# Kernel tuning notes

Hardware: AMD Instinct MI355X
Metric: run time of the kernel (lower is better)

## Reference

```python
import jax, jax.numpy as jnp
import numpy as np

TEMPERATURE = 0.07

def l2norm(x, eps=1e-12):
    # torch.nn.functional.normalize(dim=1): x / max(||x||, eps)
    n = jnp.sqrt(jnp.sum(x * x, axis=1, keepdims=True))
    return x / jnp.maximum(n, eps)

def setup_inputs() -> dict:
    key = jax.random.key(0)
    ks = jax.random.split(key, 8)
    B, D_in, H, M, Q, NNEG = 1024, 2048, 1024, 256, 65536, 16384
    return {
        "y1": jax.random.normal(ks[0], (B, D_in), dtype=jnp.float32),
        "y2": jax.random.normal(ks[1], (B, D_in), dtype=jnp.float32),
        "W_enc_q": jax.random.normal(ks[2], (D_in, H), dtype=jnp.float32) * 0.02,
        "W_enc_k": jax.random.normal(ks[3], (D_in, H), dtype=jnp.float32) * 0.02,
        "W_proj": jax.random.normal(ks[4], (H, M), dtype=jnp.float32) * 0.02,
        "queue": jax.random.normal(ks[5], (Q, M), dtype=jnp.float32),
        "sample_idx": jax.random.randint(ks[6], (NNEG,), 0, Q, dtype=jnp.int32),
        "write_idx": jnp.arange(B, dtype=jnp.int32),
    }

def reference(y1, y2, W_enc_q, W_enc_k, W_proj, queue, sample_idx, write_idx):
    # query path (trainable)
    q = l2norm((y2 @ W_enc_q) @ W_proj)                 # [B, M]
    # key path (no_grad in original)
    k = jax.lax.stop_gradient(l2norm((y1 @ W_enc_k) @ W_proj))  # [B, M]
    # sample negatives from GPU-resident queue (gather) + normalize
    neg = l2norm(queue[sample_idx])                     # [NNEG, M]
    pos_logits = jnp.sum(q * k, axis=1, keepdims=True)  # [B, 1]
    neg_logits = q @ neg.T                              # [B, NNEG]
    logits = jnp.concatenate([pos_logits, neg_logits], axis=1) / TEMPERATURE
    # cross_entropy with labels == 0
    loss = -jnp.mean(jax.nn.log_softmax(logits, axis=-1)[:, 0])
    # FIFO append modeled as circular-buffer scatter write
    new_queue = queue.at[write_idx].set(k)
    return loss, new_queue
```

## Files before the change

### kernel.cpp

```cpp
#include <hip/hip_runtime.h>
#include <hip/hip_bf16.h>
#include <math.h>
#include <stdint.h>


typedef __attribute__((ext_vector_type(4))) float floatx4;
typedef __attribute__((ext_vector_type(8))) short bf16x8;
typedef __attribute__((ext_vector_type(8))) unsigned short ushort8;

#define BM 128
#define BN 128
#define BK 32

__device__ __forceinline__ unsigned short f2bf(float x) {
    union { float f; unsigned int u; } v; v.f = x;
    unsigned int r = v.u + 0x7FFFu + ((v.u >> 16) & 1u);
    return (unsigned short)(r >> 16);
}

__device__ __forceinline__ void async_cp16(const void* g, void* l) {
    auto gp = reinterpret_cast<const __attribute__((address_space(1))) unsigned int*>(
        reinterpret_cast<uintptr_t>(g));
    auto lp = reinterpret_cast<__attribute__((address_space(3))) unsigned int*>(
        reinterpret_cast<uintptr_t>(l));
    __builtin_amdgcn_global_load_lds(gp, lp, 16, 0, 0);
}

__global__ __launch_bounds__(256) void copy_f4(const float4* __restrict__ in,
                                               float4* __restrict__ out, int n4) {
    int i = blockIdx.x * 256 + threadIdx.x;
    int stride = gridDim.x * 256;
    for (; i < n4; i += stride) out[i] = in[i];
}

__global__ __launch_bounds__(256) void cast_bf16(const float* __restrict__ in,
                                                 unsigned short* __restrict__ out,
                                                 long n) {
    long i = (long)blockIdx.x * 256 + threadIdx.x;
    const float4* in4 = (const float4*)in;
    float4 a = in4[i * 2], b = in4[i * 2 + 1];
    ushort8 o;
    o[0] = f2bf(a.x); o[1] = f2bf(a.y); o[2] = f2bf(a.z); o[3] = f2bf(a.w);
    o[4] = f2bf(b.x); o[5] = f2bf(b.y); o[6] = f2bf(b.z); o[7] = f2bf(b.w);
    ((ushort8*)out)[i] = o;
}

__global__ __launch_bounds__(256) void transpose_cast(const float* __restrict__ in,
                                                      unsigned short* __restrict__ out,
                                                      int R, int C) {
    __shared__ unsigned short tile[32][33];
    int c0 = blockIdx.x * 32, r0 = blockIdx.y * 32;
    int tx = threadIdx.x & 31, ty = threadIdx.x >> 5;
#pragma unroll
    for (int i = 0; i < 4; ++i)
        tile[ty + i * 8][tx] = f2bf(in[(size_t)(r0 + ty + i * 8) * C + c0 + tx]);
    __syncthreads();
#pragma unroll
    for (int i = 0; i < 4; ++i)
        out[(size_t)(c0 + ty + i * 8) * R + r0 + tx] = tile[tx][ty + i * 8];
}

__global__ __launch_bounds__(256) void gemm_nt(const unsigned short* __restrict__ Ag,
                                               const unsigned short* __restrict__ Bg,
                                               float* __restrict__ Cg,
                                               int M_, int N_, int K_, int nsplit,
                                               long sAb, long sBb) {
    __shared__ unsigned short As[BM * BK];
    __shared__ unsigned short Bs[BN * BK];
    const int z = blockIdx.z;
    const int batch = z / nsplit, split = z - batch * nsplit;
    const unsigned short* A = Ag + (long)batch * sAb;
    const unsigned short* B = Bg + (long)batch * sBb;
    float* C = Cg + (long)z * M_ * N_;
    const int Kc = K_ / nsplit;
    const int kbeg = split * Kc;
    const int row0 = blockIdx.y * BM, col0 = blockIdx.x * BN;
    const int t = threadIdx.x;
    const int wave = t >> 6, lane = t & 63;
    const int wr = wave >> 1, wc = wave & 1;
    const int lrow = lane & 15, quad = lane >> 4;

    floatx4 acc[4][4] = {};

    for (int kk = kbeg; kk < kbeg + Kc; kk += BK) {
#pragma unroll
        for (int r = 0; r < 2; ++r) {
            int c = t + r * 256;
            int arow = c >> 2, aoff = (c & 3) * 8;
            async_cp16(A + (size_t)(row0 + arow) * K_ + kk + aoff,
                       (char*)As + (size_t)c * 16);
            async_cp16(B + (size_t)(col0 + arow) * K_ + kk + aoff,
                       (char*)Bs + (size_t)c * 16);
        }
        __syncthreads();
        bf16x8 af[4], bfr[4];
#pragma unroll
        for (int i = 0; i < 4; ++i) {
            af[i]  = *(const bf16x8*)(As + (size_t)(wr * 64 + i * 16 + lrow) * BK + quad * 8);
            bfr[i] = *(const bf16x8*)(Bs + (size_t)(wc * 64 + i * 16 + lrow) * BK + quad * 8);
        }
#pragma unroll
        for (int i = 0; i < 4; ++i)
#pragma unroll
            for (int j = 0; j < 4; ++j)
                acc[i][j] = __builtin_amdgcn_mfma_f32_16x16x32_bf16(af[i], bfr[j], acc[i][j], 0, 0, 0);
        __syncthreads();
    }
#pragma unroll
    for (int i = 0; i < 4; ++i) {
        int grow = row0 + wr * 64 + i * 16 + quad * 4;
#pragma unroll
        for (int j = 0; j < 4; ++j) {
            int gcol = col0 + wc * 64 + j * 16 + lrow;
#pragma unroll
            for (int r = 0; r < 4; ++r)
                C[(size_t)(grow + r) * N_ + gcol] = acc[i][j][r];
        }
    }
}

__global__ __launch_bounds__(256) void reduce2_cast(const float* __restrict__ P,
                                                    unsigned short* __restrict__ out,
                                                    long BH) {
    long i = ((long)blockIdx.x * 256 + threadIdx.x) * 8;
    long batch = (i >= BH) ? 1 : 0;
    long j = i - batch * BH;
    const float* p0 = P + batch * 2 * BH + j;
    const float* p1 = p0 + BH;
    float4 a0 = *(const float4*)p0, a1 = *(const float4*)(p0 + 4);
    float4 b0 = *(const float4*)p1, b1 = *(const float4*)(p1 + 4);
    ushort8 o;
    o[0] = f2bf(a0.x + b0.x); o[1] = f2bf(a0.y + b0.y);
    o[2] = f2bf(a0.z + b0.z); o[3] = f2bf(a0.w + b0.w);
    o[4] = f2bf(a1.x + b1.x); o[5] = f2bf(a1.y + b1.y);
    o[6] = f2bf(a1.z + b1.z); o[7] = f2bf(a1.w + b1.w);
    *(ushort8*)(out + i) = o;
}

__global__ __launch_bounds__(256) void qk_finalize(const float* __restrict__ P,
                                                   const int* __restrict__ widx,
                                                   unsigned short* __restrict__ qkb,
                                                   float* __restrict__ newq,
                                                   float* __restrict__ pos,
                                                   float* __restrict__ sumexp,
                                                   int B_, int nsplit, float invT) {
    const int i = blockIdx.x, t = threadIdx.x;
    const long RM = (long)B_ * 256;
    float sq = 0.f, sk = 0.f;
    for (int s = 0; s < nsplit; ++s) {
        sq += P[(long)s * RM + (long)i * 256 + t];
        sk += P[(long)(nsplit + s) * RM + (long)i * 256 + t];
    }
    __shared__ float r0[256], r1[256], r2[256];
    r0[t] = sq * sq; r1[t] = sk * sk; r2[t] = sq * sk;
    __syncthreads();
    for (int off = 128; off > 0; off >>= 1) {
        if (t < off) { r0[t] += r0[t + off]; r1[t] += r1[t + off]; r2[t] += r2[t + off]; }
        __syncthreads();
    }
    float nq = fmaxf(sqrtf(r0[0]), 1e-12f);
    float nk = fmaxf(sqrtf(r1[0]), 1e-12f);
    float qn = sq / nq, kn = sk / nk;
    qkb[(size_t)i * 256 + t] = f2bf(qn);
    qkb[(size_t)(B_ + i) * 256 + t] = f2bf(kn);
    newq[(size_t)widx[i] * 256 + t] = kn;
    if (t == 0) {
        float p = (r2[0] / (nq * nk)) * invT;
        pos[i] = p;
        sumexp[i] = __expf(p);
    }
}

__global__ __launch_bounds__(256) void gather_norm(const float* __restrict__ queue,
                                                   const int* __restrict__ sidx,
                                                   unsigned short* __restrict__ neg) {
    const int r = blockIdx.x * 4 + (threadIdx.x >> 6);
    const int lane = threadIdx.x & 63;
    const float4* src = (const float4*)(queue + (size_t)sidx[r] * 256);
    float4 v = src[lane];
    float ss = v.x * v.x + v.y * v.y + v.z * v.z + v.w * v.w;
#pragma unroll
    for (int off = 1; off < 64; off <<= 1) ss += __shfl_xor(ss, off);
    float inv = 1.f / fmaxf(sqrtf(ss), 1e-12f);
    ushort8 dummy; (void)dummy;
    unsigned short o[4] = { f2bf(v.x * inv), f2bf(v.y * inv),
                            f2bf(v.z * inv), f2bf(v.w * inv) };
    *(unsigned long long*)(neg + (size_t)r * 256 + lane * 4) =
        *(unsigned long long*)o;
}

__global__ __launch_bounds__(256) void gemm_logits(const unsigned short* __restrict__ A,
                                                   const unsigned short* __restrict__ B,
                                                   float* __restrict__ sumexp,
                                                   int N_, int K_, float invT) {
    __shared__ unsigned short As[BM * BK];
    __shared__ unsigned short Bs[BN * BK];
    __shared__ float rowred[BM];
    const int row0 = blockIdx.y * BM, col0 = blockIdx.x * BN;
    const int t = threadIdx.x;
    const int wave = t >> 6, lane = t & 63;
    const int wr = wave >> 1, wc = wave & 1;
    const int lrow = lane & 15, quad = lane >> 4;

    floatx4 acc[4][4] = {};

    for (int kk = 0; kk < K_; kk += BK) {
#pragma unroll
        for (int r = 0; r < 2; ++r) {
            int c = t + r * 256;
            int arow = c >> 2, aoff = (c & 3) * 8;
            async_cp16(A + (size_t)(row0 + arow) * K_ + kk + aoff,
                       (char*)As + (size_t)c * 16);
            async_cp16(B + (size_t)(col0 + arow) * K_ + kk + aoff,
                       (char*)Bs + (size_t)c * 16);
        }
        __syncthreads();
        bf16x8 af[4], bfr[4];
#pragma unroll
        for (int i = 0; i < 4; ++i) {
            af[i]  = *(const bf16x8*)(As + (size_t)(wr * 64 + i * 16 + lrow) * BK + quad * 8);
            bfr[i] = *(const bf16x8*)(Bs + (size_t)(wc * 64 + i * 16 + lrow) * BK + quad * 8);
        }
#pragma unroll
        for (int i = 0; i < 4; ++i)
#pragma unroll
            for (int j = 0; j < 4; ++j)
                acc[i][j] = __builtin_amdgcn_mfma_f32_16x16x32_bf16(af[i], bfr[j], acc[i][j], 0, 0, 0);
        __syncthreads();
    }
    if (t < BM) rowred[t] = 0.f;
    __syncthreads();
#pragma unroll
    for (int i = 0; i < 4; ++i) {
#pragma unroll
        for (int r = 0; r < 4; ++r) {
            float s = 0.f;
#pragma unroll
            for (int j = 0; j < 4; ++j) s += __expf(acc[i][j][r] * invT);
            s += __shfl_xor(s, 1); s += __shfl_xor(s, 2);
            s += __shfl_xor(s, 4); s += __shfl_xor(s, 8);
            if (lrow == 0) atomicAdd(&rowred[wr * 64 + i * 16 + quad * 4 + r], s);
        }
    }
    __syncthreads();
    if (t < BM) atomicAdd(&sumexp[row0 + t], rowred[t]);
}

__global__ __launch_bounds__(256) void final_loss(const float* __restrict__ pos,
                                                  const float* __restrict__ sumexp,
                                                  float* __restrict__ out, int B_) {
    const int t = threadIdx.x;
    float acc = 0.f;
    for (int i = t; i < B_; i += 256) acc += logf(sumexp[i]) - pos[i];
    __shared__ float s[256];
    s[t] = acc;
    __syncthreads();
    for (int off = 128; off > 0; off >>= 1) {
        if (t < off) s[t] += s[t + off];
        __syncthreads();
    }
    if (t == 0) out[0] = s[0] / (float)B_;
}

extern "C" void kernel_launch(void* const* d_in, const int* in_sizes, int n_in,
                              void* d_out, int out_size, void* d_ws, size_t ws_size,
                              hipStream_t stream) {
    const float* y1    = (const float*)d_in[0];
    const float* y2    = (const float*)d_in[1];
    const float* Wq    = (const float*)d_in[2];
    const float* Wk    = (const float*)d_in[3];
    const float* Wp    = (const float*)d_in[4];
    const float* queue = (const float*)d_in[5];
    const int*   sidx  = (const int*)d_in[6];
    const int*   widx  = (const int*)d_in[7];
    float* out = (float*)d_out;

    const int B    = in_sizes[7];
    const int NNEG = in_sizes[6];
    const int D    = in_sizes[0] / B;
    const int H    = in_sizes[2] / D;
    const int M    = in_sizes[4] / H;
    const int Q    = in_sizes[5] / M;
    const float invT = 1.0f / 0.07f;
    const int NS_E = 2;
    const int NS_P = 8;

    float* ws  = (float*)d_ws;
    float* Pe  = ws;
    float* Pp  = ws;
    float* pos    = Pe + (size_t)2 * NS_E * B * H;
    float* sumexp = pos + B;
    unsigned short* bs  = (unsigned short*)(sumexp + B);
    unsigned short* y2b = bs;
    unsigned short* y1b = y2b + (size_t)B * D;
    unsigned short* Wqt = y1b + (size_t)B * D;
    unsigned short* Wkt = Wqt + (size_t)H * D;
    unsigned short* Wpt = Wkt + (size_t)H * D;
    unsigned short* T1b = y2b;
    unsigned short* qkb = y1b;
    unsigned short* negb = Wqt;

    copy_f4<<<4096, 256, 0, stream>>>((const float4*)queue, (float4*)(out + 1),
                                      (int)((size_t)Q * M / 4));

    cast_bf16<<<(int)((size_t)B * D / 2048), 256, 0, stream>>>(y2, y2b, (long)B * D);
    cast_bf16<<<(int)((size_t)B * D / 2048), 256, 0, stream>>>(y1, y1b, (long)B * D);
    transpose_cast<<<dim3(H / 32, D / 32), 256, 0, stream>>>(Wq, Wqt, D, H);
    transpose_cast<<<dim3(H / 32, D / 32), 256, 0, stream>>>(Wk, Wkt, D, H);
    transpose_cast<<<dim3(M / 32, H / 32), 256, 0, stream>>>(Wp, Wpt, H, M);

    gemm_nt<<<dim3(H / BN, B / BM, 2 * NS_E), 256, 0, stream>>>(
        y2b, Wqt, Pe, B, H, D, NS_E, (long)B * D, (long)H * D);

    reduce2_cast<<<(int)((size_t)2 * B * H / 2048), 256, 0, stream>>>(
        Pe, T1b, (long)B * H);

    gather_norm<<<NNEG / 4, 256, 0, stream>>>(queue, sidx, negb);

    gemm_nt<<<dim3(M / BN, B / BM, 2 * NS_P), 256, 0, stream>>>(
        T1b, Wpt, Pp, B, M, H, NS_P, (long)B * H, 0L);

    qk_finalize<<<B, 256, 0, stream>>>(Pp, widx, qkb, out + 1, pos, sumexp,
                                       B, NS_P, invT);

    gemm_logits<<<dim3(NNEG / BN, B / BM, 1), 256, 0, stream>>>(
        qkb, negb, sumexp, NNEG, M, invT);

    final_loss<<<1, 256, 0, stream>>>(pos, sumexp, out, B);
}
```

Baseline: 256.7 us.

## Fuse prep kernels into one launch, drop encoder split-K, retile GEMMs

Result: faster. 239.8 us (-6.6%).

```diff
diff --git a/kernel.cpp b/kernel.cpp
--- a/kernel.cpp
+++ b/kernel.cpp
@@ -7,10 +7,6 @@
 typedef __attribute__((ext_vector_type(4))) float floatx4;
 typedef __attribute__((ext_vector_type(8))) short bf16x8;
 typedef __attribute__((ext_vector_type(8))) unsigned short ushort8;
-
-#define BM 128
-#define BN 128
-#define BK 32
 
 __device__ __forceinline__ unsigned short f2bf(float x) {
     union { float f; unsigned int u; } v; v.f = x;
@@ -26,115 +22,191 @@
     __builtin_amdgcn_global_load_lds(gp, lp, 16, 0, 0);
 }
 
-__global__ __launch_bounds__(256) void copy_f4(const float4* __restrict__ in,
-                                               float4* __restrict__ out, int n4) {
-    int i = blockIdx.x * 256 + threadIdx.x;
-    int stride = gridDim.x * 256;
-    for (; i < n4; i += stride) out[i] = in[i];
-}
-
-__global__ __launch_bounds__(256) void cast_bf16(const float* __restrict__ in,
-                                                 unsigned short* __restrict__ out,
-                                                 long n) {
-    long i = (long)blockIdx.x * 256 + threadIdx.x;
-    const float4* in4 = (const float4*)in;
-    float4 a = in4[i * 2], b = in4[i * 2 + 1];
-    ushort8 o;
-    o[0] = f2bf(a.x); o[1] = f2bf(a.y); o[2] = f2bf(a.z); o[3] = f2bf(a.w);
-    o[4] = f2bf(b.x); o[5] = f2bf(b.y); o[6] = f2bf(b.z); o[7] = f2bf(b.w);
-    ((ushort8*)out)[i] = o;
-}
-
-__global__ __launch_bounds__(256) void transpose_cast(const float* __restrict__ in,
-                                                      unsigned short* __restrict__ out,
-                                                      int R, int C) {
+__global__ __launch_bounds__(256) void prep(
+    const float4* __restrict__ queue4, float4* __restrict__ newq4, int nCopy,
+    const float* __restrict__ y2, const float* __restrict__ y1,
+    unsigned short* __restrict__ y2b, unsigned short* __restrict__ y1b,
+    const float* __restrict__ Wq, const float* __restrict__ Wk,
+    const float* __restrict__ Wp,
+    unsigned short* __restrict__ Wqt, unsigned short* __restrict__ Wkt,
+    unsigned short* __restrict__ Wpt,
+    const float* __restrict__ queue, const int* __restrict__ sidx,
+    unsigned short* __restrict__ negb,
+    int D, int H, int M) {
     __shared__ unsigned short tile[32][33];
-    int c0 = blockIdx.x * 32, r0 = blockIdx.y * 32;
-    int tx = threadIdx.x & 31, ty = threadIdx.x >> 5;
-#pragma unroll
-    for (int i = 0; i < 4; ++i)
-        tile[ty + i * 8][tx] = f2bf(in[(size_t)(r0 + ty + i * 8) * C + c0 + tx]);
-    __syncthreads();
-#pragma unroll
-    for (int i = 0; i < 4; ++i)
-        out[(size_t)(c0 + ty + i * 8) * R + r0 + tx] = tile[tx][ty + i * 8];
-}
-
-__global__ __launch_bounds__(256) void gemm_nt(const unsigned short* __restrict__ Ag,
-                                               const unsigned short* __restrict__ Bg,
-                                               float* __restrict__ Cg,
-                                               int M_, int N_, int K_, int nsplit,
-                                               long sAb, long sBb) {
-    __shared__ unsigned short As[BM * BK];
-    __shared__ unsigned short Bs[BN * BK];
+    const int b = blockIdx.x, t = threadIdx.x;
+    const int nCastY = 1024;
+    const int nTW = (D / 32) * (H / 32);
+    const int nTWp = (H / 32) * (M / 32);
+
+    if (b < nCopy) {
+        int base = b * 1024 + t;
+#pragma unroll
+        for (int i = 0; i < 4; ++i) newq4[base + i * 256] = queue4[base + i * 256];
+        return;
+    }
+    int bb = b - nCopy;
+    if (bb < 2 * nCastY) {
+        const float* in = (bb < nCastY) ? y2 : y1;
+        unsigned short* outp = (bb < nCastY) ? y2b : y1b;
+        long i = (long)(bb % nCastY) * 256 + t;
+        const float4* in4 = (const float4*)in;
+        float4 a = in4[i * 2], c = in4[i * 2 + 1];
+        ushort8 o;
+        o[0] = f2bf(a.x); o[1] = f2bf(a.y); o[2] = f2bf(a.z); o[3] = f2bf(a.w);
+        o[4] = f2bf(c.x); o[5] = f2bf(c.y); o[6] = f2bf(c.z); o[7] = f2bf(c.w);
+        ((ushort8*)outp)[i] = o;
+        return;
+    }
+    bb -= 2 * nCastY;
+    if (bb < 2 * nTW + nTWp) {
+        const float* in; unsigned short* outp; int R, C, idx;
+        if (bb < nTW)           { in = Wq; outp = Wqt; R = D; C = H; idx = bb; }
+        else if (bb < 2 * nTW)  { in = Wk; outp = Wkt; R = D; C = H; idx = bb - nTW; }
+        else                    { in = Wp; outp = Wpt; R = H; C = M; idx = bb - 2 * nTW; }
+        int cb = C / 32;
+        int c0 = (idx % cb) * 32, r0 = (idx / cb) * 32;
+        int tx = t & 31, ty = t >> 5;
+#pragma unroll
+        for (int i = 0; i < 4; ++i)
+            tile[ty + i * 8][tx] = f2bf(in[(size_t)(r0 + ty + i * 8) * C + c0 + tx]);
+        __syncthreads();
+#pragma unroll
+        for (int i = 0; i < 4; ++i)
+            outp[(size_t)(c0 + ty + i * 8) * R + r0 + tx] = tile[tx][ty + i * 8];
+        return;
+    }
+    bb -= 2 * nTW + nTWp;
+    {
+        int r = bb * 4 + (t >> 6);
+        int lane = t & 63;
+        const float4* src = (const float4*)(queue + (size_t)sidx[r] * 256);
+        float4 v = src[lane];
+        float ss = v.x * v.x + v.y * v.y + v.z * v.z + v.w * v.w;
+#pragma unroll
+        for (int off = 1; off < 64; off <<= 1) ss += __shfl_xor(ss, off);
+        float inv = 1.f / fmaxf(sqrtf(ss), 1e-12f);
+        unsigned short o[4] = { f2bf(v.x * inv), f2bf(v.y * inv),
+                                f2bf(v.z * inv), f2bf(v.w * inv) };
+        *(unsigned long long*)(negb + (size_t)r * 256 + lane * 4) =
+            *(unsigned long long*)o;
+    }
+}
+
+__global__ __launch_bounds__(256) void gemm_enc(const unsigned short* __restrict__ Ag,
+                                                const unsigned short* __restrict__ Bg,
+                                                unsigned short* __restrict__ Cg,
+                                                int No, int Ko,
+                                                long sAb, long sBb, long sCb) {
+    __shared__ unsigned short As[128 * 32];
+    __shared__ unsigned short Bs[64 * 32];
+    const int batch = blockIdx.z;
+    const unsigned short* A = Ag + (long)batch * sAb;
+    const unsigned short* B = Bg + (long)batch * sBb;
+    unsigned short* C = Cg + (long)batch * sCb;
+    const int row0 = blockIdx.y * 128, col0 = blockIdx.x * 64;
+    const int t = threadIdx.x;
+    const int lane = t & 63, wave = t >> 6;
+    const int wr = wave >> 1, wc = wave & 1;
+    const int lrow = lane & 15, quad = lane >> 4;
+
+    floatx4 acc[4][2] = {};
+
+    for (int kk = 0; kk < Ko; kk += 32) {
+        {
+            int c0 = t, c1 = t + 256;
+            async_cp16(A + (size_t)(row0 + (c0 >> 2)) * Ko + kk + (c0 & 3) * 8,
+                       (char*)As + (size_t)c0 * 16);
+            async_cp16(A + (size_t)(row0 + (c1 >> 2)) * Ko + kk + (c1 & 3) * 8,
+                       (char*)As + (size_t)c1 * 16);
+            async_cp16(B + (size_t)(col0 + (t >> 2)) * Ko + kk + (t & 3) * 8,
+                       (char*)Bs + (size_t)t * 16);
+        }
+        __syncthreads();
+        bf16x8 af[4], bf[2];
+#pragma unroll
+        for (int i = 0; i < 4; ++i)
+            af[i] = *(const bf16x8*)(As + (size_t)(wr * 64 + i * 16 + lrow) * 32 + quad * 8);
+#pragma unroll
+        for (int j = 0; j < 2; ++j)
+            bf[j] = *(const bf16x8*)(Bs + (size_t)(wc * 32 + j * 16 + lrow) * 32 + quad * 8);
+#pragma unroll
+        for (int i = 0; i < 4; ++i)
+#pragma unroll
+            for (int j = 0; j < 2; ++j)
+                acc[i][j] = __builtin_amdgcn_mfma_f32_16x16x32_bf16(af[i], bf[j], acc[i][j], 0, 0, 0);
+        __syncthreads();
+    }
+#pragma unroll
+    for (int i = 0; i < 4; ++i) {
+        int grow = row0 + wr * 64 + i * 16 + quad * 4;
+#pragma unroll
+        for (int j = 0; j < 2; ++j) {
+            int gcol = col0 + wc * 32 + j * 16 + lrow;
+#pragma unroll
+            for (int r = 0; r < 4; ++r)
+                C[(size_t)(grow + r) * No + gcol] = f2bf(acc[i][j][r]);
+        }
+    }
+}
+
+__global__ __launch_bounds__(256) void gemm_proj(const unsigned short* __restrict__ Ag,
+                                                 const unsigned short* __restrict__ Bg,
+                                                 float* __restrict__ Pg,
+                                                 int No, int Ko, int nsplit,
+                                                 long sAb) {
+    __shared__ unsigned short As[128 * 32];
+    __shared__ unsigned short Bs[64 * 32];
     const int z = blockIdx.z;
     const int batch = z / nsplit, split = z - batch * nsplit;
     const unsigned short* A = Ag + (long)batch * sAb;
-    const unsigned short* B = Bg + (long)batch * sBb;
-    float* C = Cg + (long)z * M_ * N_;
-    const int Kc = K_ / nsplit;
-    const int kbeg = split * Kc;
-    const int row0 = blockIdx.y * BM, col0 = blockIdx.x * BN;
+    const unsigned short* B = Bg;
+    float* P = Pg + (long)z * 1024 * No;
+    const int Kc = Ko / nsplit, kbeg = split * Kc;
+    const int row0 = blockIdx.y * 128, col0 = blockIdx.x * 64;
     const int t = threadIdx.x;
-    const int wave = t >> 6, lane = t & 63;
+    const int lane = t & 63, wave = t >> 6;
     const int wr = wave >> 1, wc = wave & 1;
     const int lrow = lane & 15, quad = lane >> 4;
 
-    floatx4 acc[4][4] = {};
-
-    for (int kk = kbeg; kk < kbeg + Kc; kk += BK) {
-#pragma unroll
-        for (int r = 0; r < 2; ++r) {
-            int c = t + r * 256;
-            int arow = c >> 2, aoff = (c & 3) * 8;
-            async_cp16(A + (size_t)(row0 + arow) * K_ + kk + aoff,
-                       (char*)As + (size_t)c * 16);
-            async_cp16(B + (size_t)(col0 + arow) * K_ + kk + aoff,
-                       (char*)Bs + (size_t)c * 16);
-        }
-        __syncthreads();
-        bf16x8 af[4], bfr[4];
-#pragma unroll
-        for (int i = 0; i < 4; ++i) {
-            af[i]  = *(const bf16x8*)(As + (size_t)(wr * 64 + i * 16 + lrow) * BK + quad * 8);
-            bfr[i] = *(const bf16x8*)(Bs + (size_t)(wc * 64 + i * 16 + lrow) * BK + quad * 8);
-        }
-#pragma unroll
-        for (int i = 0; i < 4; ++i)
-#pragma unroll
-            for (int j = 0; j < 4; ++j)
-                acc[i][j] = __builtin_amdgcn_mfma_f32_16x16x32_bf16(af[i], bfr[j], acc[i][j], 0, 0, 0);
+    floatx4 acc[4][2] = {};
+
+    for (int kk = kbeg; kk < kbeg + Kc; kk += 32) {
+        {
+            int c0 = t, c1 = t + 256;
+            async_cp16(A + (size_t)(row0 + (c0 >> 2)) * Ko + kk + (c0 & 3) * 8,
+                       (char*)As + (size_t)c0 * 16);
+            async_cp16(A + (size_t)(row0 + (c1 >> 2)) * Ko + kk + (c1 & 3) * 8,
+                       (char*)As + (size_t)c1 * 16);
+            async_cp16(B + (size_t)(col0 + (t >> 2)) * Ko + kk + (t & 3) * 8,
+                       (char*)Bs + (size_t)t * 16);
+        }
+        __syncthreads();
+        bf16x8 af[4], bf[2];
+#pragma unroll
+        for (int i = 0; i < 4; ++i)
+            af[i] = *(const bf16x8*)(As + (size_t)(wr * 64 + i * 16 + lrow) * 32 + quad * 8);
+#pragma unroll
+        for (int j = 0; j < 2; ++j)
+            bf[j] = *(const bf16x8*)(Bs + (size_t)(wc * 32 + j * 16 + lrow) * 32 + quad * 8);
+#pragma unroll
+        for (int i = 0; i < 4; ++i)
+#pragma unroll
+            for (int j = 0; j < 2; ++j)
+                acc[i][j] = __builtin_amdgcn_mfma_f32_16x16x32_bf16(af[i], bf[j], acc[i][j], 0, 0, 0);
         __syncthreads();
     }
 #pragma unroll
     for (int i = 0; i < 4; ++i) {
         int grow = row0 + wr * 64 + i * 16 + quad * 4;
 #pragma unroll
-        for (int j = 0; j < 4; ++j) {
-            int gcol = col0 + wc * 64 + j * 16 + lrow;
+        for (int j = 0; j < 2; ++j) {
+            int gcol = col0 + wc * 32 + j * 16 + lrow;
 #pragma unroll
             for (int r = 0; r < 4; ++r)
-                C[(size_t)(grow + r) * N_ + gcol] = acc[i][j][r];
-        }
-    }
-}
-
-__global__ __launch_bounds__(256) void reduce2_cast(const float* __restrict__ P,
-                                                    unsigned short* __restrict__ out,
-                                                    long BH) {
-    long i = ((long)blockIdx.x * 256 + threadIdx.x) * 8;
-    long batch = (i >= BH) ? 1 : 0;
-    long j = i - batch * BH;
-    const float* p0 = P + batch * 2 * BH + j;
-    const float* p1 = p0 + BH;
-    float4 a0 = *(const float4*)p0, a1 = *(const float4*)(p0 + 4);
-    float4 b0 = *(const float4*)p1, b1 = *(const float4*)(p1 + 4);
-    ushort8 o;
-    o[0] = f2bf(a0.x + b0.x); o[1] = f2bf(a0.y + b0.y);
-    o[2] = f2bf(a0.z + b0.z); o[3] = f2bf(a0.w + b0.w);
-    o[4] = f2bf(a1.x + b1.x); o[5] = f2bf(a1.y + b1.y);
-    o[6] = f2bf(a1.z + b1.z); o[7] = f2bf(a1.w + b1.w);
-    *(ushort8*)(out + i) = o;
+                P[(size_t)(grow + r) * No + gcol] = acc[i][j][r];
+        }
+    }
 }
 
 __global__ __launch_bounds__(256) void qk_finalize(const float* __restrict__ P,
@@ -171,64 +243,49 @@
     }
 }
 
-__global__ __launch_bounds__(256) void gather_norm(const float* __restrict__ queue,
-                                                   const int* __restrict__ sidx,
-                                                   unsigned short* __restrict__ neg) {
-    const int r = blockIdx.x * 4 + (threadIdx.x >> 6);
-    const int lane = threadIdx.x & 63;
-    const float4* src = (const float4*)(queue + (size_t)sidx[r] * 256);
-    float4 v = src[lane];
-    float ss = v.x * v.x + v.y * v.y + v.z * v.z + v.w * v.w;
-#pragma unroll
-    for (int off = 1; off < 64; off <<= 1) ss += __shfl_xor(ss, off);
-    float inv = 1.f / fmaxf(sqrtf(ss), 1e-12f);
-    ushort8 dummy; (void)dummy;
-    unsigned short o[4] = { f2bf(v.x * inv), f2bf(v.y * inv),
-                            f2bf(v.z * inv), f2bf(v.w * inv) };
-    *(unsigned long long*)(neg + (size_t)r * 256 + lane * 4) =
-        *(unsigned long long*)o;
-}
-
 __global__ __launch_bounds__(256) void gemm_logits(const unsigned short* __restrict__ A,
                                                    const unsigned short* __restrict__ B,
                                                    float* __restrict__ sumexp,
-                                                   int N_, int K_, float invT) {
-    __shared__ unsigned short As[BM * BK];
-    __shared__ unsigned short Bs[BN * BK];
-    __shared__ float rowred[BM];
-    const int row0 = blockIdx.y * BM, col0 = blockIdx.x * BN;
+                                                   int Ko, float invT) {
+    __shared__ unsigned short As[128 * 64];
+    __shared__ unsigned short Bs[128 * 64];
+    __shared__ float rowred[128];
+    const int row0 = blockIdx.y * 128, col0 = blockIdx.x * 128;
     const int t = threadIdx.x;
-    const int wave = t >> 6, lane = t & 63;
+    const int lane = t & 63, wave = t >> 6;
     const int wr = wave >> 1, wc = wave & 1;
     const int lrow = lane & 15, quad = lane >> 4;
 
     floatx4 acc[4][4] = {};
 
-    for (int kk = 0; kk < K_; kk += BK) {
-#pragma unroll
-        for (int r = 0; r < 2; ++r) {
+    for (int kk = 0; kk < Ko; kk += 64) {
+#pragma unroll
+        for (int r = 0; r < 4; ++r) {
             int c = t + r * 256;
-            int arow = c >> 2, aoff = (c & 3) * 8;
-            async_cp16(A + (size_t)(row0 + arow) * K_ + kk + aoff,
+            async_cp16(A + (size_t)(row0 + (c >> 3)) * Ko + kk + (c & 7) * 8,
                        (char*)As + (size_t)c * 16);
-            async_cp16(B + (size_t)(col0 + arow) * K_ + kk + aoff,
+            async_cp16(B + (size_t)(col0 + (c >> 3)) * Ko + kk + (c & 7) * 8,
                        (char*)Bs + (size_t)c * 16);
         }
         __syncthreads();
-        bf16x8 af[4], bfr[4];
-#pragma unroll
-        for (int i = 0; i < 4; ++i) {
-            af[i]  = *(const bf16x8*)(As + (size_t)(wr * 64 + i * 16 + lrow) * BK + quad * 8);
-            bfr[i] = *(const bf16x8*)(Bs + (size_t)(wc * 64 + i * 16 + lrow) * BK + quad * 8);
-        }
-#pragma unroll
-        for (int i = 0; i < 4; ++i)
-#pragma unroll
-            for (int j = 0; j < 4; ++j)
-                acc[i][j] = __builtin_amdgcn_mfma_f32_16x16x32_bf16(af[i], bfr[j], acc[i][j], 0, 0, 0);
-        __syncthreads();
-    }
-    if (t < BM) rowred[t] = 0.f;
+        bf16x8 af[4][2], bf[4][2];
+#pragma unroll
+        for (int i = 0; i < 4; ++i)
+#pragma unroll
+            for (int k2 = 0; k2 < 2; ++k2) {
+                af[i][k2] = *(const bf16x8*)(As + (size_t)(wr * 64 + i * 16 + lrow) * 64 + k2 * 32 + quad * 8);
+                bf[i][k2] = *(const bf16x8*)(Bs + (size_t)(wc * 64 + i * 16 + lrow) * 64 + k2 * 32 + quad * 8);
+            }
+#pragma unroll
+        for (int k2 = 0; k2 < 2; ++k2)
+#pragma unroll
+            for (int i = 0; i < 4; ++i)
+#pragma unroll
+                for (int j = 0; j < 4; ++j)
+                    acc[i][j] = __builtin_amdgcn_mfma_f32_16x16x32_bf16(af[i][k2], bf[j][k2], acc[i][j], 0, 0, 0);
+        __syncthreads();
+    }
+    if (t < 128) rowred[t] = 0.f;
     __syncthreads();
 #pragma unroll
     for (int i = 0; i < 4; ++i) {
@@ -243,7 +300,7 @@
         }
     }
     __syncthreads();
-    if (t < BM) atomicAdd(&sumexp[row0 + t], rowred[t]);
+    if (t < 128) atomicAdd(&sumexp[row0 + t], rowred[t]);
 }
 
 __global__ __launch_bounds__(256) void final_loss(const float* __restrict__ pos,
@@ -282,49 +339,40 @@
     const int M    = in_sizes[4] / H;
     const int Q    = in_sizes[5] / M;
     const float invT = 1.0f / 0.07f;
-    const int NS_E = 2;
-    const int NS_P = 8;
+    const int NS_P = 4;
 
     float* ws  = (float*)d_ws;
-    float* Pe  = ws;
-    float* Pp  = ws;
-    float* pos    = Pe + (size_t)2 * NS_E * B * H;
+    float* Pp     = ws;
+    float* pos    = Pp + (size_t)2 * NS_P * B * M;
     float* sumexp = pos + B;
-    unsigned short* bs  = (unsigned short*)(sumexp + B);
-    unsigned short* y2b = bs;
-    unsigned short* y1b = y2b + (size_t)B * D;
-    unsigned short* Wqt = y1b + (size_t)B * D;
-    unsigned short* Wkt = Wqt + (size_t)H * D;
-    unsigned short* Wpt = Wkt + (size_t)H * D;
-    unsigned short* T1b = y2b;
-    unsigned short* qkb = y1b;
-    unsigned short* negb = Wqt;
-
-    copy_f4<<<4096, 256, 0, stream>>>((const float4*)queue, (float4*)(out + 1),
-                                      (int)((size_t)Q * M / 4));
-
-    cast_bf16<<<(int)((size_t)B * D / 2048), 256, 0, stream>>>(y2, y2b, (long)B * D);
-    cast_bf16<<<(int)((size_t)B * D / 2048), 256, 0, stream>>>(y1, y1b, (long)B * D);
-    transpose_cast<<<dim3(H / 32, D / 32), 256, 0, stream>>>(Wq, Wqt, D, H);
-    transpose_cast<<<dim3(H / 32, D / 32), 256, 0, stream>>>(Wk, Wkt, D, H);
-    transpose_cast<<<dim3(M / 32, H / 32), 256, 0, stream>>>(Wp, Wpt, H, M);
-
-    gemm_nt<<<dim3(H / BN, B / BM, 2 * NS_E), 256, 0, stream>>>(
-        y2b, Wqt, Pe, B, H, D, NS_E, (long)B * D, (long)H * D);
-
-    reduce2_cast<<<(int)((size_t)2 * B * H / 2048), 256, 0, stream>>>(
-        Pe, T1b, (long)B * H);
-
-    gather_norm<<<NNEG / 4, 256, 0, stream>>>(queue, sidx, negb);
-
-    gemm_nt<<<dim3(M / BN, B / BM, 2 * NS_P), 256, 0, stream>>>(
-        T1b, Wpt, Pp, B, M, H, NS_P, (long)B * H, 0L);
+    unsigned short* us = (unsigned short*)(sumexp + B);
+    unsigned short* y2b  = us;
+    unsigned short* y1b  = y2b + (size_t)B * D;
+    unsigned short* Wqt  = y1b + (size_t)B * D;
+    unsigned short* Wkt  = Wqt + (size_t)H * D;
+    unsigned short* Wpt  = Wkt + (size_t)H * D;
+    unsigned short* T12b = Wpt + (size_t)M * H;
+    unsigned short* qkb  = T12b + (size_t)2 * B * H;
+    unsigned short* negb = qkb + (size_t)2 * B * M;
+
+    const int nCopy = (int)((size_t)Q * M / 4 / 1024);
+    const int nPrep = nCopy + 2 * 1024 + 2 * (D / 32) * (H / 32)
+                    + (H / 32) * (M / 32) + NNEG / 4;
+    prep<<<nPrep, 256, 0, stream>>>((const float4*)queue, (float4*)(out + 1), nCopy,
+                                    y2, y1, y2b, y1b, Wq, Wk, Wp, Wqt, Wkt, Wpt,
+                                    queue, sidx, negb, D, H, M);
+
+    gemm_enc<<<dim3(H / 64, B / 128, 2), 256, 0, stream>>>(
+        y2b, Wqt, T12b, H, D, (long)B * D, (long)H * D, (long)B * H);
+
+    gemm_proj<<<dim3(M / 64, B / 128, 2 * NS_P), 256, 0, stream>>>(
+        T12b, Wpt, Pp, M, H, NS_P, (long)B * H);
 
     qk_finalize<<<B, 256, 0, stream>>>(Pp, widx, qkb, out + 1, pos, sumexp,
                                        B, NS_P, invT);
 
-    gemm_logits<<<dim3(NNEG / BN, B / BM, 1), 256, 0, stream>>>(
-        qkb, negb, sumexp, NNEG, M, invT);
+    gemm_logits<<<dim3(NNEG / 128, B / 128), 256, 0, stream>>>(
+        qkb, negb, sumexp, M, invT);
 
     final_loss<<<1, 256, 0, stream>>>(pos, sumexp, out, B);
 }
```
